# Kernel tuning notes

Hardware: AMD Instinct MI355X
Metric: run time of the kernel (lower is better)

## Reference

```python
import jax, jax.numpy as jnp
import numpy as np
from jax import lax

B = 4096
SRC = 50   # source_seq_len (encoder runs SRC-1 steps)
TGT = 25   # target_seq_len
R = 1024   # rnn_size
H = 67     # HUMAN_SIZE
I = 82     # input_size = 67 + 15 one-hot actions


def gru_cell(x, h, Wi, Wh, bi, bh):
    # torch.nn.GRUCell semantics; gate order (r, z, n); Wi:[3R,in], Wh:[3R,R]
    gi = x @ Wi.T + bi
    gh = h @ Wh.T + bh
    ir, iz, inn = jnp.split(gi, 3, axis=1)
    hr, hz, hn = jnp.split(gh, 3, axis=1)
    r = jax.nn.sigmoid(ir + hr)
    z = jax.nn.sigmoid(iz + hz)
    n = jnp.tanh(inn + r * hn)
    return (1.0 - z) * n + z * h


def setup_inputs() -> dict:
    key = jax.random.key(0)
    ks = jax.random.split(key, 12)
    s = 0.05
    return {
        "encoder_inputs": jax.random.normal(ks[0], (B, SRC - 1, I), jnp.float32),
        "decoder_inputs": jax.random.normal(ks[1], (B, TGT, I), jnp.float32),
        "Wi1": jax.random.normal(ks[2], (3 * R, I), jnp.float32) * s,
        "Wh1": jax.random.normal(ks[3], (3 * R, R), jnp.float32) * s,
        "bi1": jax.random.normal(ks[4], (3 * R,), jnp.float32) * s,
        "bh1": jax.random.normal(ks[5], (3 * R,), jnp.float32) * s,
        "Wi2": jax.random.normal(ks[6], (3 * R, R), jnp.float32) * s,
        "Wh2": jax.random.normal(ks[7], (3 * R, R), jnp.float32) * s,
        "bi2": jax.random.normal(ks[8], (3 * R,), jnp.float32) * s,
        "bh2": jax.random.normal(ks[9], (3 * R,), jnp.float32) * s,
        "Wfc": jax.random.normal(ks[10], (H, 2 * R), jnp.float32) * s,
        "bfc": jax.random.normal(ks[11], (H,), jnp.float32) * s,
        "use_cuda": 0,
    }


def reference(encoder_inputs, decoder_inputs, Wi1, Wh1, bi1, bh1,
              Wi2, Wh2, bi2, bh2, Wfc, bfc, use_cuda):
    # dropout=0.0 / eval mode -> dropout is identity (faithful to module defaults)
    bsz = encoder_inputs.shape[0]
    enc = jnp.transpose(encoder_inputs, (1, 0, 2))  # [SRC-1, B, I]
    dec = jnp.transpose(decoder_inputs, (1, 0, 2))  # [TGT,   B, I]

    s1 = jnp.zeros((bsz, R), encoder_inputs.dtype)
    s2 = jnp.zeros((bsz, R), encoder_inputs.dtype)

    def enc_step(carry, x):
        s1, s2 = carry
        s1 = gru_cell(x, s1, Wi1, Wh1, bi1, bh1)
        s2 = gru_cell(s1, s2, Wi2, Wh2, bi2, bh2)
        return (s1, s2), None

    (s1, s2), _ = lax.scan(enc_step, (s1, s2), enc)

    # decoder feeds back previous output (loop_function = identity on prev)
    prev0 = dec[0][:, :H]

    def dec_step(carry, dec_t):
        s1, s2, prev = carry
        inp = lax.stop_gradient(jnp.concatenate([prev, dec_t[:, H:]], axis=1))  # .detach()
        s1 = gru_cell(inp, s1, Wi1, Wh1, bi1, bh1)
        s2 = gru_cell(s1, s2, Wi2, Wh2, bi2, bh2)
        state_out = jnp.concatenate([s1, s2], axis=1)          # [B, 2R]
        out = inp[:, :H] + state_out @ Wfc.T + bfc             # residual velocities
        return (s1, s2, out), out

    _, outputs = lax.scan(dec_step, (s1, s2, prev0), dec)      # [TGT, B, H]
    return jnp.transpose(outputs, (1, 0, 2))                   # [B, TGT, H]
```

## Files before the change

### kernel.cpp

```cpp
#include <hip/hip_runtime.h>
#include <hip/hip_bf16.h>
#include <math.h>

#define B_        4096
#define ENC_STEPS 49
#define TGT_      25
#define R_        1024
#define H_        67
#define I_        82
#define IP_       96
#define IP2_      192
#define NG_       3072
#define FCN_      128
#define K2_       2048

typedef unsigned short u16;
typedef __attribute__((ext_vector_type(8))) short bf16x8_t;
typedef __attribute__((ext_vector_type(4))) float f32x4_t;

__device__ __forceinline__ float bf2f(u16 h) {
    union { unsigned int u; float f; } v; v.u = ((unsigned int)h) << 16; return v.f;
}
__device__ __forceinline__ u16 f2bf(float f) {
    union { unsigned int u; float f; } v; v.f = f;
    unsigned int u = v.u;
    u += 0x7fffu + ((u >> 16) & 1u);
    return (u16)(u >> 16);
}
__device__ __forceinline__ float sigmf(float x) { return 1.f / (1.f + __expf(-x)); }
__device__ __forceinline__ float tanhfast(float x) { return 1.f - 2.f / (__expf(2.f * x) + 1.f); }

__device__ __forceinline__ void g2l16(const u16* g, u16* l) {
    __builtin_amdgcn_global_load_lds(
        (const __attribute__((address_space(1))) unsigned int*)(const void*)g,
        (__attribute__((address_space(3))) unsigned int*)(void*)l,
        16, 0, 0);
}

__global__ void cast_bf16_kernel(const float* __restrict__ s, u16* __restrict__ d, int n) {
    int i = blockIdx.x * 256 + threadIdx.x;
    if (i < n) d[i] = f2bf(s[i]);
}
__global__ void pad_wi1_dup_kernel(const float* __restrict__ s, u16* __restrict__ d) {
    int i = blockIdx.x * 256 + threadIdx.x;
    if (i >= NG_ * IP2_) return;
    int r = i / IP2_, c = i % IP2_;
    int cc = (c < IP_) ? c : c - IP_;
    d[i] = (cc < I_) ? f2bf(s[r * I_ + cc]) : (u16)0;
}
__global__ void pad_wfc_kernel(const float* __restrict__ s, u16* __restrict__ d) {
    int i = blockIdx.x * 256 + threadIdx.x;
    if (i >= FCN_ * K2_) return;
    int r = i / K2_, c = i % K2_;
    d[i] = (r < H_) ? f2bf(s[r * K2_ + c]) : (u16)0;
}

__global__ void pad_all_x_kernel(const float* __restrict__ enc, u16* __restrict__ xall) {
    int i = blockIdx.x * 256 + threadIdx.x;
    if (i >= B_ * ENC_STEPS * IP_) return;
    int c = i % IP_;
    int t = (i / IP_) % ENC_STEPS;
    int b = i / (IP_ * ENC_STEPS);
    float v = (c < I_) ? enc[((size_t)b * ENC_STEPS + t) * I_ + c] : 0.f;
    u16 hi = f2bf(v);
    u16 lo = f2bf(v - bf2f(hi));
    size_t base = ((size_t)t * B_ + b) * IP2_;
    xall[base + c]       = hi;
    xall[base + IP_ + c] = lo;
}

__global__ void build_inp_kernel(const float* __restrict__ prev, int pstride,
                                 const float* __restrict__ dec, int t,
                                 u16* __restrict__ xpad) {
    int i = blockIdx.x * 256 + threadIdx.x;
    if (i >= B_ * IP_) return;
    int b = i / IP_, c = i % IP_;
    float v = 0.f;
    if (c < H_)      v = prev[(size_t)b * pstride + c];
    else if (c < I_) v = dec[((size_t)b * TGT_ + t) * I_ + c];
    u16 hi = f2bf(v);
    u16 lo = f2bf(v - bf2f(hi));
    xpad[(size_t)b * IP2_ + c]       = hi;
    xpad[(size_t)b * IP2_ + IP_ + c] = lo;
}

template<int KX>
__global__ __launch_bounds__(256, 2) void gru_step_kernel(
    const u16* __restrict__ Ax, int ldax,
    const u16* __restrict__ Wx,
    const u16* __restrict__ Ah, int ldah,
    const u16* __restrict__ Wh,
    const float* __restrict__ bi, const float* __restrict__ bh,
    float* __restrict__ hf,
    u16* __restrict__ hout)
{
    __shared__ __align__(16) u16 As[2][128 * 64];
    __shared__ __align__(16) u16 Ws[2][3 * 64 * 64];

    const int tid  = threadIdx.x;
    const int lane = tid & 63, wave = tid >> 6;
    const int wm = wave >> 1, wn = wave & 1;
    const int mbase = blockIdx.y * 128;
    const int nbase = blockIdx.x * 64;
    const int lr = lane & 15;
    const int swkey = lr & 7;

    constexpr int NX = KX / 64;
    constexpr int NH = R_ / 64;
    constexpr int NT = NX + NH;

    f32x4_t acc_r[4][2], acc_z[4][2], acc_xn[4][2], acc_hn[4][2];
#pragma unroll
    for (int i = 0; i < 4; i++)
#pragma unroll
        for (int j = 0; j < 2; j++) {
            acc_r[i][j]  = (f32x4_t){0,0,0,0};
            acc_z[i][j]  = (f32x4_t){0,0,0,0};
            acc_xn[i][j] = (f32x4_t){0,0,0,0};
            acc_hn[i][j] = (f32x4_t){0,0,0,0};
        }

    auto stage = [&](int s, int b) {
        const u16* A; int lda; const u16* W; int ldw; int k0;
        if (s < NX) { A = Ax; lda = ldax; W = Wx; ldw = KX; k0 = s * 64; }
        else        { A = Ah; lda = ldah; W = Wh; ldw = R_;  k0 = (s - NX) * 64; }
#pragma unroll
        for (int p = 0; p < 4; p++) {
            int g = tid + p * 256;
            int row = g >> 3;
            int ch  = (g & 7) ^ (row & 7);
            g2l16(A + (size_t)(mbase + row) * lda + k0 + ch * 8, As[b] + g * 8);
        }
#pragma unroll
        for (int p = 0; p < 6; p++) {
            int q = tid + p * 256;
            int row = q >> 3;
            int gate = row >> 6, rg = row & 63;
            int cw = (q & 7) ^ (row & 7);
            g2l16(W + ((size_t)gate * R_ + nbase + rg) * ldw + k0 + cw * 8, Ws[b] + q * 8);
        }
    };

    auto compute = [&](bool xpass, int b) {
#pragma unroll
        for (int kk = 0; kk < 2; kk++) {
            const int pos = ((kk * 4 + (lane >> 4)) ^ swkey) * 8;
            bf16x8_t a_f[4], w_r[2], w_z[2], w_n[2];
#pragma unroll
            for (int i = 0; i < 4; i++)
                a_f[i] = *(const bf16x8_t*)(As[b] + (wm * 64 + i * 16 + lr) * 64 + pos);
#pragma unroll
            for (int j = 0; j < 2; j++) {
                int c = wn * 32 + j * 16 + lr;
                w_r[j] = *(const bf16x8_t*)(Ws[b] + c * 64 + pos);
                w_z[j] = *(const bf16x8_t*)(Ws[b] + (64 + c) * 64 + pos);
                w_n[j] = *(const bf16x8_t*)(Ws[b] + (128 + c) * 64 + pos);
            }
            __builtin_amdgcn_s_setprio(1);
#pragma unroll
            for (int i = 0; i < 4; i++)
#pragma unroll
                for (int j = 0; j < 2; j++) {
                    acc_r[i][j] = __builtin_amdgcn_mfma_f32_16x16x32_bf16(a_f[i], w_r[j], acc_r[i][j], 0, 0, 0);
                    acc_z[i][j] = __builtin_amdgcn_mfma_f32_16x16x32_bf16(a_f[i], w_z[j], acc_z[i][j], 0, 0, 0);
                }
            if (xpass) {
#pragma unroll
                for (int i = 0; i < 4; i++)
#pragma unroll
                    for (int j = 0; j < 2; j++)
                        acc_xn[i][j] = __builtin_amdgcn_mfma_f32_16x16x32_bf16(a_f[i], w_n[j], acc_xn[i][j], 0, 0, 0);
            } else {
#pragma unroll
                for (int i = 0; i < 4; i++)
#pragma unroll
                    for (int j = 0; j < 2; j++)
                        acc_hn[i][j] = __builtin_amdgcn_mfma_f32_16x16x32_bf16(a_f[i], w_n[j], acc_hn[i][j], 0, 0, 0);
            }
            __builtin_amdgcn_s_setprio(0);
        }
    };

    stage(0, 0);
    stage(1, 1);
#pragma unroll 1
    for (int s = 0; s < NT; ++s) {
        if (s + 1 < NT) asm volatile("s_waitcnt vmcnt(10)" ::: "memory");
        else            asm volatile("s_waitcnt vmcnt(0)" ::: "memory");
        __builtin_amdgcn_s_barrier();
        __builtin_amdgcn_sched_barrier(0);
        compute(s < NX, s & 1);
        __builtin_amdgcn_s_barrier();
        __builtin_amdgcn_sched_barrier(0);
        if (s + 2 < NT) stage(s + 2, s & 1);
    }

    const int rr2 = (lane >> 4) * 4;
#pragma unroll
    for (int j = 0; j < 2; j++) {
        const int col = nbase + wn * 32 + j * 16 + lr;
        const float b_ir = bi[col],          b_hr = bh[col];
        const float b_iz = bi[R_ + col],     b_hz = bh[R_ + col];
        const float b_in = bi[2 * R_ + col], b_hn = bh[2 * R_ + col];
#pragma unroll
        for (int i = 0; i < 4; i++) {
#pragma unroll
            for (int r = 0; r < 4; r++) {
                const int row = mbase + wm * 64 + i * 16 + rr2 + r;
                const float hold = hf[(size_t)row * R_ + col];
                const float rv = sigmf(acc_r[i][j][r] + b_ir + b_hr);
                const float zv = sigmf(acc_z[i][j][r] + b_iz + b_hz);
                const float nv = tanhfast(acc_xn[i][j][r] + b_in + rv * (acc_hn[i][j][r] + b_hn));
                const float hn = (1.f - zv) * nv + zv * hold;
                hf[(size_t)row * R_ + col] = hn;
                hout[(size_t)row * K2_ + col] = f2bf(hn);
            }
        }
    }
}

__global__ __launch_bounds__(256) void fc_part_kernel(
    const u16* __restrict__ A, const u16* __restrict__ W, float* __restrict__ part) {
    __shared__ __align__(16) u16 As[64 * 32];
    __shared__ __align__(16) u16 Bs[128 * 32];
    const int tid  = threadIdx.x;
    const int lane = tid & 63, wave = tid >> 6;
    const int wm = wave >> 1, wn = wave & 1;
    const int mbase = blockIdx.y * 64;
    const int kbase = blockIdx.x * 512;
    const int lr = lane & 15;
    const int sw = (((lane >> 4) ^ ((lr >> 1) & 3)) * 8);

    f32x4_t acc[2][4];
#pragma unroll
    for (int i = 0; i < 2; i++)
#pragma unroll
        for (int j = 0; j < 4; j++) acc[i][j] = (f32x4_t){0, 0, 0, 0};

    for (int k0 = 0; k0 < 512; k0 += 32) {
        __syncthreads();
        {
            int g = tid;
            int row = g >> 2;
            int ch  = (g & 3) ^ ((row >> 1) & 3);
            g2l16(A + (size_t)(mbase + row) * K2_ + kbase + k0 + ch * 8, As + g * 8);
        }
#pragma unroll
        for (int p = 0; p < 2; p++) {
            int q = tid + p * 256;
            int row = q >> 2;
            int cw  = (q & 3) ^ ((row >> 1) & 3);
            g2l16(W + (size_t)row * K2_ + kbase + k0 + cw * 8, Bs + q * 8);
        }
        __syncthreads();
        bf16x8_t a_f[2], b_f[4];
#pragma unroll
        for (int i = 0; i < 2; i++)
            a_f[i] = *(const bf16x8_t*)(As + (wm * 32 + i * 16 + lr) * 32 + sw);
#pragma unroll
        for (int j = 0; j < 4; j++)
            b_f[j] = *(const bf16x8_t*)(Bs + (wn * 64 + j * 16 + lr) * 32 + sw);
#pragma unroll
        for (int i = 0; i < 2; i++)
#pragma unroll
            for (int j = 0; j < 4; j++)
                acc[i][j] = __builtin_amdgcn_mfma_f32_16x16x32_bf16(a_f[i], b_f[j], acc[i][j], 0, 0, 0);
    }
    const int rr2 = (lane >> 4) * 4;
#pragma unroll
    for (int i = 0; i < 2; i++)
#pragma unroll
        for (int r = 0; r < 4; r++) {
            int row = mbase + wm * 32 + i * 16 + rr2 + r;
#pragma unroll
            for (int j = 0; j < 4; j++) {
                int col = wn * 64 + j * 16 + lr;
                part[((size_t)blockIdx.x * B_ + row) * FCN_ + col] = acc[i][j][r];
            }
        }
}

__global__ void fc_finish_kernel(const float* __restrict__ part, const float* __restrict__ prev,
                                 int pstride, const float* __restrict__ bfc,
                                 float* __restrict__ out, int t,
                                 const float* __restrict__ dec, u16* __restrict__ xpad,
                                 int write_x) {
    int i = blockIdx.x * 256 + threadIdx.x;
    if (i >= B_ * IP_) return;
    int b = i / IP_, c = i % IP_;
    float v = 0.f;
    if (c < H_) {
        size_t idx = (size_t)b * FCN_ + c;
        const size_t S = (size_t)B_ * FCN_;
        float s = (part[idx] + part[S + idx]) + (part[2 * S + idx] + part[3 * S + idx]);
        v = prev[(size_t)b * pstride + c] + s + bfc[c];
        out[((size_t)b * TGT_ + t) * H_ + c] = v;
    } else if (c < I_ && write_x) {
        v = dec[((size_t)b * TGT_ + (t + 1)) * I_ + c];
    }
    if (write_x) {
        u16 hi = f2bf(v);
        u16 lo = f2bf(v - bf2f(hi));
        xpad[(size_t)b * IP2_ + c]       = hi;
        xpad[(size_t)b * IP2_ + IP_ + c] = lo;
    }
}

extern "C" void kernel_launch(void* const* d_in, const int* in_sizes, int n_in,
                              void* d_out, int out_size, void* d_ws, size_t ws_size,
                              hipStream_t stream) {
    (void)in_sizes; (void)n_in; (void)out_size; (void)ws_size;
    const float* enc = (const float*)d_in[0];
    const float* dec = (const float*)d_in[1];
    const float* Wi1 = (const float*)d_in[2];
    const float* Wh1 = (const float*)d_in[3];
    const float* bi1 = (const float*)d_in[4];
    const float* bh1 = (const float*)d_in[5];
    const float* Wi2 = (const float*)d_in[6];
    const float* Wh2 = (const float*)d_in[7];
    const float* bi2 = (const float*)d_in[8];
    const float* bh2 = (const float*)d_in[9];
    const float* Wfc = (const float*)d_in[10];
    const float* bfc = (const float*)d_in[11];
    float* out = (float*)d_out;

    char* ws = (char*)d_ws;
    size_t off = 0;
    auto alloc = [&](size_t bytes) -> char* {
        char* p = ws + off;
        off += (bytes + 255) & ~(size_t)255;
        return p;
    };
    u16* Wh1b  = (u16*)alloc((size_t)NG_ * R_ * 2);
    u16* Wi2b  = (u16*)alloc((size_t)NG_ * R_ * 2);
    u16* Wh2b  = (u16*)alloc((size_t)NG_ * R_ * 2);
    u16* Wi1pb = (u16*)alloc((size_t)NG_ * IP2_ * 2);
    u16* Wfcb  = (u16*)alloc((size_t)FCN_ * K2_ * 2);
    u16* sbuf0 = (u16*)alloc((size_t)B_ * K2_ * 2);
    float* s1f = (float*)alloc((size_t)B_ * R_ * 4);
    float* s2f = (float*)alloc((size_t)B_ * R_ * 4);
    u16* sbuf1 = (u16*)alloc((size_t)B_ * K2_ * 2);
    u16* xall  = (u16*)alloc((size_t)ENC_STEPS * B_ * IP2_ * 2);
    u16* xpad2 = (u16*)alloc((size_t)B_ * IP2_ * 2);
    float* cfcp = (float*)alloc((size_t)4 * B_ * FCN_ * 4);
    u16* sbuf[2] = { sbuf0, sbuf1 };

    hipMemsetAsync(sbuf0, 0,
                   (size_t)B_ * K2_ * 2 + 2 * (size_t)B_ * R_ * 4, stream);

    cast_bf16_kernel<<<(NG_ * R_ + 255) / 256, 256, 0, stream>>>(Wh1, Wh1b, NG_ * R_);
    cast_bf16_kernel<<<(NG_ * R_ + 255) / 256, 256, 0, stream>>>(Wi2, Wi2b, NG_ * R_);
    cast_bf16_kernel<<<(NG_ * R_ + 255) / 256, 256, 0, stream>>>(Wh2, Wh2b, NG_ * R_);
    pad_wi1_dup_kernel<<<(NG_ * IP2_ + 255) / 256, 256, 0, stream>>>(Wi1, Wi1pb);
    pad_wfc_kernel<<<(FCN_ * K2_ + 255) / 256, 256, 0, stream>>>(Wfc, Wfcb);
    pad_all_x_kernel<<<(B_ * ENC_STEPS * IP_ + 255) / 256, 256, 0, stream>>>(enc, xall);

    dim3 gru_grid(R_ / 64, B_ / 128, 1);
    dim3 fc_grid(4, B_ / 64, 1);
    const int binp_blocks = (B_ * IP_ + 255) / 256;
    const int fcf_blocks  = (B_ * IP_ + 255) / 256;

    int phase = 0;

    for (int t = 0; t < ENC_STEPS; t++) {
        u16* cur = sbuf[phase];
        u16* nxt = sbuf[phase ^ 1];
        gru_step_kernel<IP2_><<<gru_grid, 256, 0, stream>>>(
            xall + (size_t)t * B_ * IP2_, IP2_, Wi1pb,
            cur, K2_, Wh1b, bi1, bh1, s1f, nxt);
        gru_step_kernel<R_><<<gru_grid, 256, 0, stream>>>(
            nxt, K2_, Wi2b,
            cur + R_, K2_, Wh2b, bi2, bh2, s2f, nxt + R_);
        phase ^= 1;
    }

    build_inp_kernel<<<binp_blocks, 256, 0, stream>>>(dec, TGT_ * I_, dec, 0, xpad2);
    for (int t = 0; t < TGT_; t++) {
        const float* prev;
        int pstride;
        if (t == 0) { prev = dec;                 pstride = TGT_ * I_; }
        else        { prev = out + (t - 1) * H_;  pstride = TGT_ * H_; }
        u16* cur = sbuf[phase];
        u16* nxt = sbuf[phase ^ 1];
        gru_step_kernel<IP2_><<<gru_grid, 256, 0, stream>>>(
            xpad2, IP2_, Wi1pb,
            cur, K2_, Wh1b, bi1, bh1, s1f, nxt);
        gru_step_kernel<R_><<<gru_grid, 256, 0, stream>>>(
            nxt, K2_, Wi2b,
            cur + R_, K2_, Wh2b, bi2, bh2, s2f, nxt + R_);
        fc_part_kernel<<<fc_grid, 256, 0, stream>>>(nxt, Wfcb, cfcp);
        fc_finish_kernel<<<fcf_blocks, 256, 0, stream>>>(
            cfcp, prev, pstride, bfc, out, t, dec, xpad2, (t < TGT_ - 1) ? 1 : 0);
        phase ^= 1;
    }
}
```

Baseline: 7.832 ms.

## Split GRU gate MFMA phases with barrier interleaving and precompute load offsets

Precomputes per-thread global and LDS offsets for the A and W tile loads so the staging loop does less address arithmetic. Breaks each k-substep into three gate phases (r, z, n). Each phase loads only two W fragments, then runs a barrier, an lgkmcnt wait and an MFMA burst, which aims to stagger waves and cut register pressure. This adds six extra barriers per k-substep and drops the sched_barrier fences, which risks more synchronisation stalls and less overlap of LDS reads with MFMA.

```diff
diff --git a/kernel.cpp b/kernel.cpp
--- a/kernel.cpp
+++ b/kernel.cpp
@@ -109,6 +109,30 @@
     constexpr int NH = R_ / 64;
     constexpr int NT = NX + NH;
 
+    int offAx[4], offAh[4], offWx[6], offWh[6], ldsA[4], ldsW[6];
+#pragma unroll
+    for (int p = 0; p < 4; p++) {
+        int g = tid + p * 256, row = g >> 3, ch = (g & 7) ^ (row & 7);
+        offAx[p] = (mbase + row) * ldax + ch * 8;
+        offAh[p] = (mbase + row) * ldah + ch * 8;
+        ldsA[p]  = g * 8;
+    }
+#pragma unroll
+    for (int p = 0; p < 6; p++) {
+        int q = tid + p * 256, row = q >> 3;
+        int gate = row >> 6, rg = row & 63, cw = (q & 7) ^ (row & 7);
+        offWx[p] = (gate * R_ + nbase + rg) * KX + cw * 8;
+        offWh[p] = (gate * R_ + nbase + rg) * R_ + cw * 8;
+        ldsW[p]  = q * 8;
+    }
+    int aro[4], wro[3][2];
+#pragma unroll
+    for (int i = 0; i < 4; i++) aro[i] = (wm * 64 + i * 16 + lr) * 64;
+#pragma unroll
+    for (int g = 0; g < 3; g++)
+#pragma unroll
+        for (int j = 0; j < 2; j++) wro[g][j] = (g * 64 + wn * 32 + j * 16 + lr) * 64;
+
     f32x4_t acc_r[4][2], acc_z[4][2], acc_xn[4][2], acc_hn[4][2];
 #pragma unroll
     for (int i = 0; i < 4; i++)
@@ -121,63 +145,76 @@
         }
 
     auto stage = [&](int s, int b) {
-        const u16* A; int lda; const u16* W; int ldw; int k0;
-        if (s < NX) { A = Ax; lda = ldax; W = Wx; ldw = KX; k0 = s * 64; }
-        else        { A = Ah; lda = ldah; W = Wh; ldw = R_;  k0 = (s - NX) * 64; }
-#pragma unroll
-        for (int p = 0; p < 4; p++) {
-            int g = tid + p * 256;
-            int row = g >> 3;
-            int ch  = (g & 7) ^ (row & 7);
-            g2l16(A + (size_t)(mbase + row) * lda + k0 + ch * 8, As[b] + g * 8);
-        }
-#pragma unroll
-        for (int p = 0; p < 6; p++) {
-            int q = tid + p * 256;
-            int row = q >> 3;
-            int gate = row >> 6, rg = row & 63;
-            int cw = (q & 7) ^ (row & 7);
-            g2l16(W + ((size_t)gate * R_ + nbase + rg) * ldw + k0 + cw * 8, Ws[b] + q * 8);
+        if (s < NX) {
+            const u16* A = Ax + s * 64;
+            const u16* W = Wx + s * 64;
+#pragma unroll
+            for (int p = 0; p < 4; p++) g2l16(A + offAx[p], As[b] + ldsA[p]);
+#pragma unroll
+            for (int p = 0; p < 6; p++) g2l16(W + offWx[p], Ws[b] + ldsW[p]);
+        } else {
+            const u16* A = Ah + (s - NX) * 64;
+            const u16* W = Wh + (s - NX) * 64;
+#pragma unroll
+            for (int p = 0; p < 4; p++) g2l16(A + offAh[p], As[b] + ldsA[p]);
+#pragma unroll
+            for (int p = 0; p < 6; p++) g2l16(W + offWh[p], Ws[b] + ldsW[p]);
         }
     };
 
-    auto compute = [&](bool xpass, int b) {
+    auto tile = [&](bool xpass, int b) {
+        const u16* Ab = As[b];
+        const u16* Wb = Ws[b];
 #pragma unroll
         for (int kk = 0; kk < 2; kk++) {
             const int pos = ((kk * 4 + (lane >> 4)) ^ swkey) * 8;
-            bf16x8_t a_f[4], w_r[2], w_z[2], w_n[2];
-#pragma unroll
-            for (int i = 0; i < 4; i++)
-                a_f[i] = *(const bf16x8_t*)(As[b] + (wm * 64 + i * 16 + lr) * 64 + pos);
-#pragma unroll
-            for (int j = 0; j < 2; j++) {
-                int c = wn * 32 + j * 16 + lr;
-                w_r[j] = *(const bf16x8_t*)(Ws[b] + c * 64 + pos);
-                w_z[j] = *(const bf16x8_t*)(Ws[b] + (64 + c) * 64 + pos);
-                w_n[j] = *(const bf16x8_t*)(Ws[b] + (128 + c) * 64 + pos);
-            }
+            bf16x8_t a_f[4], w0, w1;
+#pragma unroll
+            for (int i = 0; i < 4; i++) a_f[i] = *(const bf16x8_t*)(Ab + aro[i] + pos);
+            w0 = *(const bf16x8_t*)(Wb + wro[0][0] + pos);
+            w1 = *(const bf16x8_t*)(Wb + wro[0][1] + pos);
+            __builtin_amdgcn_s_barrier();
+            asm volatile("s_waitcnt lgkmcnt(0)" ::: "memory");
             __builtin_amdgcn_s_setprio(1);
 #pragma unroll
-            for (int i = 0; i < 4; i++)
-#pragma unroll
-                for (int j = 0; j < 2; j++) {
-                    acc_r[i][j] = __builtin_amdgcn_mfma_f32_16x16x32_bf16(a_f[i], w_r[j], acc_r[i][j], 0, 0, 0);
-                    acc_z[i][j] = __builtin_amdgcn_mfma_f32_16x16x32_bf16(a_f[i], w_z[j], acc_z[i][j], 0, 0, 0);
-                }
-            if (xpass) {
-#pragma unroll
-                for (int i = 0; i < 4; i++)
-#pragma unroll
-                    for (int j = 0; j < 2; j++)
-                        acc_xn[i][j] = __builtin_amdgcn_mfma_f32_16x16x32_bf16(a_f[i], w_n[j], acc_xn[i][j], 0, 0, 0);
-            } else {
-#pragma unroll
-                for (int i = 0; i < 4; i++)
-#pragma unroll
-                    for (int j = 0; j < 2; j++)
-                        acc_hn[i][j] = __builtin_amdgcn_mfma_f32_16x16x32_bf16(a_f[i], w_n[j], acc_hn[i][j], 0, 0, 0);
+            for (int i = 0; i < 4; i++) {
+                acc_r[i][0] = __builtin_amdgcn_mfma_f32_16x16x32_bf16(a_f[i], w0, acc_r[i][0], 0, 0, 0);
+                acc_r[i][1] = __builtin_amdgcn_mfma_f32_16x16x32_bf16(a_f[i], w1, acc_r[i][1], 0, 0, 0);
             }
             __builtin_amdgcn_s_setprio(0);
+            __builtin_amdgcn_s_barrier();
+            w0 = *(const bf16x8_t*)(Wb + wro[1][0] + pos);
+            w1 = *(const bf16x8_t*)(Wb + wro[1][1] + pos);
+            __builtin_amdgcn_s_barrier();
+            asm volatile("s_waitcnt lgkmcnt(0)" ::: "memory");
+            __builtin_amdgcn_s_setprio(1);
+#pragma unroll
+            for (int i = 0; i < 4; i++) {
+                acc_z[i][0] = __builtin_amdgcn_mfma_f32_16x16x32_bf16(a_f[i], w0, acc_z[i][0], 0, 0, 0);
+                acc_z[i][1] = __builtin_amdgcn_mfma_f32_16x16x32_bf16(a_f[i], w1, acc_z[i][1], 0, 0, 0);
+            }
+            __builtin_amdgcn_s_setprio(0);
+            __builtin_amdgcn_s_barrier();
+            w0 = *(const bf16x8_t*)(Wb + wro[2][0] + pos);
+            w1 = *(const bf16x8_t*)(Wb + wro[2][1] + pos);
+            __builtin_amdgcn_s_barrier();
+            asm volatile("s_waitcnt lgkmcnt(0)" ::: "memory");
+            __builtin_amdgcn_s_setprio(1);
+            if (xpass) {
+#pragma unroll
+                for (int i = 0; i < 4; i++) {
+                    acc_xn[i][0] = __builtin_amdgcn_mfma_f32_16x16x32_bf16(a_f[i], w0, acc_xn[i][0], 0, 0, 0);
+                    acc_xn[i][1] = __builtin_amdgcn_mfma_f32_16x16x32_bf16(a_f[i], w1, acc_xn[i][1], 0, 0, 0);
+                }
+            } else {
+#pragma unroll
+                for (int i = 0; i < 4; i++) {
+                    acc_hn[i][0] = __builtin_amdgcn_mfma_f32_16x16x32_bf16(a_f[i], w0, acc_hn[i][0], 0, 0, 0);
+                    acc_hn[i][1] = __builtin_amdgcn_mfma_f32_16x16x32_bf16(a_f[i], w1, acc_hn[i][1], 0, 0, 0);
+                }
+            }
+            __builtin_amdgcn_s_setprio(0);
+            __builtin_amdgcn_s_barrier();
         }
     };
 
@@ -188,10 +225,7 @@
         if (s + 1 < NT) asm volatile("s_waitcnt vmcnt(10)" ::: "memory");
         else            asm volatile("s_waitcnt vmcnt(0)" ::: "memory");
         __builtin_amdgcn_s_barrier();
-        __builtin_amdgcn_sched_barrier(0);
-        compute(s < NX, s & 1);
-        __builtin_amdgcn_s_barrier();
-        __builtin_amdgcn_sched_barrier(0);
+        tile(s < NX, s & 1);
         if (s + 2 < NT) stage(s + 2, s & 1);
     }
 
```

Result: slower. 21.66 ms (+176.6%).
